# Performance work log

Measured on AMD Instinct MI355X. Metric: run time of the kernel, lower is better.

The kernel has to match this reference:

```python
import jax, jax.numpy as jnp
import numpy as np

N_NODES = 50000
EPS = 1e-5


def _gcn_edges(edge_index, num_nodes):
    # Add self loops (PyG GCNConv default) and compute symmetric normalization.
    src = jnp.concatenate([edge_index[0], jnp.arange(num_nodes, dtype=edge_index.dtype)])
    dst = jnp.concatenate([edge_index[1], jnp.arange(num_nodes, dtype=edge_index.dtype)])
    deg = jax.ops.segment_sum(jnp.ones_like(dst, dtype=jnp.float32), dst, num_segments=num_nodes)
    dinv = jnp.where(deg > 0, jax.lax.rsqrt(deg), 0.0)
    norm = dinv[src] * dinv[dst]  # [E+N]
    return src, dst, norm


def gcn_conv(x, W, b, src, dst, norm, num_nodes):
    xw = x @ W  # [N, out]
    msg = xw[src] * norm[:, None]  # [E+N, out] gather + scale
    out = jax.ops.segment_sum(msg, dst, num_segments=num_nodes)  # scatter-add
    return out + b


def layer_norm(x, g, b):
    mu = jnp.mean(x, axis=-1, keepdims=True)
    var = jnp.mean(jnp.square(x - mu), axis=-1, keepdims=True)
    return (x - mu) * jax.lax.rsqrt(var + EPS) * g + b


def setup_inputs() -> dict:
    key = jax.random.key(0)
    ks = jax.random.split(key, 12)
    d_in, d_h, d_out = 128, 128, 64
    n_edges = 800000
    x = jax.random.normal(ks[0], (N_NODES, d_in), dtype=jnp.float32)
    edge_index = jax.random.randint(ks[1], (2, n_edges), 0, N_NODES, dtype=jnp.int64)
    s = 1.0 / np.sqrt(d_in)
    return {
        "x": x,
        "edge_index": edge_index,
        "W1": jax.random.uniform(ks[2], (d_in, d_h), jnp.float32, -s, s),
        "b1": jnp.zeros((d_h,), jnp.float32),
        "W2": jax.random.uniform(ks[3], (d_h, d_h), jnp.float32, -s, s),
        "b2": jnp.zeros((d_h,), jnp.float32),
        "W3": jax.random.uniform(ks[4], (d_h, d_out), jnp.float32, -s, s),
        "b3": jnp.zeros((d_out,), jnp.float32),
        "g1": jnp.ones((d_h,), jnp.float32),
        "be1": jnp.zeros((d_h,), jnp.float32),
        "g2": jnp.ones((d_h,), jnp.float32),
        "be2": jnp.zeros((d_h,), jnp.float32),
    }


def reference(x, edge_index, W1, b1, W2, b2, W3, b3, g1, be1, g2, be2):
    num_nodes = x.shape[0]
    src, dst, norm = _gcn_edges(edge_index, num_nodes)
    h = jax.nn.relu(gcn_conv(x, W1, b1, src, dst, norm, num_nodes))
    h = layer_norm(h, g1, be1)  # dropout is identity in eval mode
    h = jax.nn.relu(gcn_conv(h, W2, b2, src, dst, norm, num_nodes))
    h = layer_norm(h, g2, be2)
    return gcn_conv(h, W3, b3, src, dst, norm, num_nodes)
```

## Files before the change

kernel.cpp:

```cpp
#include <hip/hip_runtime.h>

#define EPSV 1e-5f

typedef _Float16 half2_t __attribute__((ext_vector_type(2)));
typedef _Float16 half8_t __attribute__((ext_vector_type(8)));
typedef float float4_t __attribute__((ext_vector_type(4)));


__global__ __launch_bounds__(256) void k_fill(const int* __restrict__ src,
                                              const int* __restrict__ dst,
                                              int* __restrict__ cursor,
                                              int* __restrict__ csr, int E, int N) {
  int slice = blockIdx.x & 7;
  int lo = (int)(((long long)N * slice) >> 3);
  int hi = (int)(((long long)N * (slice + 1)) >> 3);
  int r = (blockIdx.x >> 3) * blockDim.x + threadIdx.x;
  int stride = (gridDim.x >> 3) * blockDim.x;
  for (int e = r; e < E; e += stride) {
    int d = __builtin_nontemporal_load(&dst[e]);
    if (d >= lo && d < hi) {
      int s = __builtin_nontemporal_load(&src[e]);
      int pos = atomicAdd(&cursor[d], 1);
      if (pos < 128) csr[((size_t)d << 7) + pos] = s;
    }
  }
}


__global__ __launch_bounds__(256) void k_prep(const int* __restrict__ cursor,
                                              int* __restrict__ csr,
                                              float* __restrict__ dinv,
                                              _Float16* __restrict__ ys_y,
                                              _Float16* __restrict__ ys3,
                                              int N, int N1) {
  int i = blockIdx.x * 256 + threadIdx.x;
  if (i < N) {
    int cnt = min(cursor[i], 128);
    dinv[i] = rsqrtf((float)(cnt + 1));
    int cr = (cnt + 15) & ~15;
    for (int p = cnt; p < cr; p++) csr[((size_t)i << 7) + p] = N;
  }
  if (i < 64) {
    ((half2_t*)ys_y)[((size_t)(i >> 4) * N1 + N) * 16 + (i & 15)] = (half2_t){0, 0};
  } else if (i < 96) {
    int j = i - 64;
    ((half2_t*)ys3)[((size_t)(j >> 4) * N1 + N) * 16 + (j & 15)] = (half2_t){0, 0};
  }
}


__global__ __launch_bounds__(256) void k_wprep_all(
    const float* __restrict__ W1, const float* __restrict__ W2,
    const float* __restrict__ W3, _Float16* __restrict__ Wh1,
    _Float16* __restrict__ Wh2, _Float16* __restrict__ Wh3) {
  int bid = blockIdx.x;
  const float* W;
  _Float16* Wh;
  int COLS, t;
  if (bid < 8) { W = W1; Wh = Wh1; COLS = 128; t = bid * 256 + threadIdx.x; }
  else if (bid < 16) { W = W2; Wh = Wh2; COLS = 128; t = (bid - 8) * 256 + threadIdx.x; }
  else { W = W3; Wh = Wh3; COLS = 64; t = (bid - 16) * 256 + threadIdx.x; }
  int NT = (COLS / 16) * 4 * 64;
  if (t >= NT) return;
  int lane = t & 63;
  int ks = (t >> 6) & 3;
  int nb = t >> 8;
  int col = nb * 16 + (lane & 15);
  int k0 = ks * 32 + (lane >> 4) * 8;
  half8_t v;
#pragma unroll
  for (int j = 0; j < 8; j++) v[j] = (_Float16)W[(size_t)(k0 + j) * COLS + col];
  *(half8_t*)&Wh[(size_t)t * 8] = v;
}


template <int COLS, bool LN, typename AT>
__global__ __launch_bounds__(256) void k_gemm_mfma(
    const AT* __restrict__ A, const float2* __restrict__ lnp,
    const float* __restrict__ g, const float* __restrict__ be,
    const _Float16* __restrict__ Wh, const float* __restrict__ dinv,
    _Float16* __restrict__ out, int N, int N1) {
  constexpr int NB = COLS / 16;
  int lane = threadIdx.x & 63;
  int w = threadIdx.x >> 6;
  int quad = lane >> 4;
  int mrow = blockIdx.x * 64 + w * 16 + (lane & 15);
  half8_t af[4];
  if (mrow < N) {
    if constexpr (LN) {
      float P = 0.f, Q = 0.f;
#pragma unroll
      for (int s = 0; s < 4; s++) {
        float2 pq = lnp[(size_t)s * N + mrow];
        P += pq.x; Q += pq.y;
      }
      float mean = P * (1.f / 128.f);
      float rstd = rsqrtf(Q * (1.f / 128.f) - mean * mean + EPSV);
#pragma unroll
      for (int ks = 0; ks < 4; ks++) {
        half8_t sv = *(const half8_t*)&A[((size_t)ks * N1 + mrow) * 32 + quad * 8];
        float4 g0 = *(const float4*)&g[ks * 32 + quad * 8];
        float4 g1 = *(const float4*)&g[ks * 32 + quad * 8 + 4];
        float4 e0 = *(const float4*)&be[ks * 32 + quad * 8];
        float4 e1 = *(const float4*)&be[ks * 32 + quad * 8 + 4];
        af[ks][0] = (_Float16)fmaf(((float)sv[0] - mean) * rstd, g0.x, e0.x);
        af[ks][1] = (_Float16)fmaf(((float)sv[1] - mean) * rstd, g0.y, e0.y);
        af[ks][2] = (_Float16)fmaf(((float)sv[2] - mean) * rstd, g0.z, e0.z);
        af[ks][3] = (_Float16)fmaf(((float)sv[3] - mean) * rstd, g0.w, e0.w);
        af[ks][4] = (_Float16)fmaf(((float)sv[4] - mean) * rstd, g1.x, e1.x);
        af[ks][5] = (_Float16)fmaf(((float)sv[5] - mean) * rstd, g1.y, e1.y);
        af[ks][6] = (_Float16)fmaf(((float)sv[6] - mean) * rstd, g1.z, e1.z);
        af[ks][7] = (_Float16)fmaf(((float)sv[7] - mean) * rstd, g1.w, e1.w);
      }
    } else {
      const AT* ap = A + (size_t)mrow * 128 + quad * 8;
#pragma unroll
      for (int ks = 0; ks < 4; ks++) {
        float4 f0 = *(const float4*)(ap + ks * 32);
        float4 f1 = *(const float4*)(ap + ks * 32 + 4);
        af[ks][0] = (_Float16)f0.x; af[ks][1] = (_Float16)f0.y;
        af[ks][2] = (_Float16)f0.z; af[ks][3] = (_Float16)f0.w;
        af[ks][4] = (_Float16)f1.x; af[ks][5] = (_Float16)f1.y;
        af[ks][6] = (_Float16)f1.z; af[ks][7] = (_Float16)f1.w;
      }
    }
  } else {
#pragma unroll
    for (int ks = 0; ks < 4; ks++)
#pragma unroll
      for (int j = 0; j < 8; j++) af[ks][j] = (_Float16)0.f;
  }
  float4_t acc[NB];
#pragma unroll
  for (int nb = 0; nb < NB; nb++) acc[nb] = (float4_t){0.f, 0.f, 0.f, 0.f};
#pragma unroll
  for (int nb = 0; nb < NB; nb++) {
#pragma unroll
    for (int ks = 0; ks < 4; ks++) {
      half8_t bf = *(const half8_t*)&Wh[(size_t)((nb * 4 + ks) * 64 + lane) * 8];
      acc[nb] = __builtin_amdgcn_mfma_f32_16x16x32_f16(af[ks], bf, acc[nb], 0, 0, 0);
    }
  }
  int orow0 = blockIdx.x * 64 + w * 16 + quad * 4;
#pragma unroll
  for (int r = 0; r < 4; r++) {
    int row = orow0 + r;
    if (row < N) {
      float dv = dinv[row];
#pragma unroll
      for (int nb = 0; nb < NB; nb++) {
        int dim = nb * 16 + (lane & 15);
        out[((size_t)(dim >> 5) * N1 + row) * 32 + (dim & 31)] =
            (_Float16)(acc[nb][r] * dv);
      }
    }
  }
}


__global__ __launch_bounds__(256) void k_aggs(
    const _Float16* __restrict__ ysrc, const int* __restrict__ csr,
    const int* __restrict__ cursor, const float* __restrict__ dinv,
    const float* __restrict__ b, _Float16* __restrict__ sdst,
    float2* __restrict__ lnp, int N, int N1) {
  int slice = blockIdx.x & 3;
  int lane = threadIdx.x & 63;
  int g = lane >> 4, li = lane & 15;
  int node = (blockIdx.x >> 2) * 16 + (threadIdx.x >> 6) * 4 + g;
  const half2_t* yb = (const half2_t*)ysrc + (size_t)slice * N1 * 16;
  int cnt = 0;
  if (node < N) cnt = min(cursor[node], 128);
  int cround = (cnt + 15) & ~15;
  size_t bin = (size_t)node << 7;
  float a0 = 0.f, a1 = 0.f;
  for (int c = 0; c < cround; c += 16) {
    int idx = csr[bin + c + li];
#pragma unroll
    for (int e = 0; e < 16; e++) {
      int s = __shfl(idx, (g << 4) | e, 64);
      half2_t u = yb[(size_t)s * 16 + li];
      a0 += (float)u[0];
      a1 += (float)u[1];
    }
  }
  half2_t us = yb[(size_t)min(node, N) * 16 + li];
  a0 += (float)us[0];
  a1 += (float)us[1];
  float di = (node < N) ? dinv[node] : 0.f;
  float2 bb = ((const float2*)b)[slice * 16 + li];
  float v0 = fmaxf(fmaf(a0, di, bb.x), 0.f);
  float v1 = fmaxf(fmaf(a1, di, bb.y), 0.f);
  float p = v0 + v1, q = fmaf(v0, v0, v1 * v1);
#pragma unroll
  for (int o = 1; o < 16; o <<= 1) {
    p += __shfl_xor(p, o, 64);
    q += __shfl_xor(q, o, 64);
  }
  if (node < N) {
    if (li == 0) lnp[(size_t)slice * N + node] = make_float2(p, q);
    half2_t o2;
    o2[0] = (_Float16)v0;
    o2[1] = (_Float16)v1;
    ((half2_t*)sdst)[((size_t)slice * N1 + node) * 16 + li] = o2;
  }
}


__global__ __launch_bounds__(256) void k_agg_out(
    const _Float16* __restrict__ ysrc, const int* __restrict__ csr,
    const int* __restrict__ cursor, const float* __restrict__ dinv,
    const float* __restrict__ b, float* __restrict__ out, int N, int N1) {
  int slice = blockIdx.x & 1;
  int lane = threadIdx.x & 63;
  int g = lane >> 4, li = lane & 15;
  int node = (blockIdx.x >> 1) * 16 + (threadIdx.x >> 6) * 4 + g;
  const half2_t* yb = (const half2_t*)ysrc + (size_t)slice * N1 * 16;
  int cnt = 0;
  if (node < N) cnt = min(cursor[node], 128);
  int cround = (cnt + 15) & ~15;
  size_t bin = (size_t)node << 7;
  float a0 = 0.f, a1 = 0.f;
  for (int c = 0; c < cround; c += 16) {
    int idx = csr[bin + c + li];
#pragma unroll
    for (int e = 0; e < 16; e++) {
      int s = __shfl(idx, (g << 4) | e, 64);
      half2_t u = yb[(size_t)s * 16 + li];
      a0 += (float)u[0];
      a1 += (float)u[1];
    }
  }
  if (node < N) {
    half2_t us = yb[(size_t)node * 16 + li];
    a0 += (float)us[0];
    a1 += (float)us[1];
    float di = dinv[node];
    float2 bb = ((const float2*)b)[slice * 16 + li];
    float2 o;
    o.x = fmaf(a0, di, bb.x);
    o.y = fmaf(a1, di, bb.y);
    ((float2*)out)[(size_t)node * 32 + slice * 16 + li] = o;
  }
}


extern "C" void kernel_launch(void* const* d_in, const int* in_sizes, int n_in,
                              void* d_out, int out_size, void* d_ws, size_t ws_size,
                              hipStream_t stream) {
  const float* x = (const float*)d_in[0];
  const int* ei = (const int*)d_in[1];
  const float* W1 = (const float*)d_in[2];
  const float* b1 = (const float*)d_in[3];
  const float* W2 = (const float*)d_in[4];
  const float* b2 = (const float*)d_in[5];
  const float* W3 = (const float*)d_in[6];
  const float* b3 = (const float*)d_in[7];
  const float* g1 = (const float*)d_in[8];
  const float* be1 = (const float*)d_in[9];
  const float* g2 = (const float*)d_in[10];
  const float* be2 = (const float*)d_in[11];

  int N = in_sizes[0] / 128;
  int E = in_sizes[1] / 2;
  int N1 = N + 1;
  const int* srcs = ei;
  const int* dsts = ei + E;

  char* ws = (char*)d_ws;
  size_t off = 0;
  auto alloc = [&](size_t bytes) -> char* {
    char* p = ws + off;
    off = (off + bytes + 255) & ~(size_t)255;
    return p;
  };
  float* dinv = (float*)alloc((size_t)N * 4);
  int* cursor = (int*)alloc((size_t)N * 4);
  int* csr = (int*)alloc((size_t)N * 128 * 4);
  _Float16* ys_y = (_Float16*)alloc((size_t)4 * N1 * 32 * 2);
  _Float16* ys_s = (_Float16*)alloc((size_t)4 * N1 * 32 * 2);
  _Float16* ys3 = (_Float16*)alloc((size_t)2 * N1 * 32 * 2);
  float2* lnp = (float2*)alloc((size_t)4 * N * 8);
  _Float16* Wh1 = (_Float16*)alloc(128 * 128 * 2);
  _Float16* Wh2 = (_Float16*)alloc(128 * 128 * 2);
  _Float16* Wh3 = (_Float16*)alloc(128 * 64 * 2);

  hipMemsetAsync(cursor, 0, (size_t)N * sizeof(int), stream);
  k_fill<<<2048, 256, 0, stream>>>(srcs, dsts, cursor, csr, E, N);
  k_prep<<<(N + 255) / 256, 256, 0, stream>>>(cursor, csr, dinv, ys_y, ys3, N, N1);
  k_wprep_all<<<20, 256, 0, stream>>>(W1, W2, W3, Wh1, Wh2, Wh3);

  int gb = (N + 63) / 64;
  int nb16 = (N + 15) / 16;

  k_gemm_mfma<128, false, float><<<gb, 256, 0, stream>>>(
      x, nullptr, nullptr, nullptr, Wh1, dinv, ys_y, N, N1);
  k_aggs<<<nb16 * 4, 256, 0, stream>>>(ys_y, csr, cursor, dinv, b1, ys_s, lnp, N, N1);
  k_gemm_mfma<128, true, _Float16><<<gb, 256, 0, stream>>>(
      ys_s, lnp, g1, be1, Wh2, dinv, ys_y, N, N1);
  k_aggs<<<nb16 * 4, 256, 0, stream>>>(ys_y, csr, cursor, dinv, b2, ys_s, lnp, N, N1);
  k_gemm_mfma<64, true, _Float16><<<gb, 256, 0, stream>>>(
      ys_s, lnp, g2, be2, Wh3, dinv, ys3, N, N1);
  k_agg_out<<<nb16 * 2, 256, 0, stream>>>(ys3, csr, cursor, dinv, b3,
                                          (float*)d_out, N, N1);
}
```

Baseline: 263.7 us.

## Merge prep kernels into fill and first GEMM; recompute dinv from counts

Folds the weight-conversion kernel into the CSR fill kernel and folds the padding/prep kernel into the first GEMM launch as extra blocks, cutting two launches. The dinv array is removed, and each consumer recomputes rsqrt(count+1) from the cursor array instead of loading a stored value. This trades launch overhead and one small array write/read for a little extra ALU work. There is a subtle risk: the first GEMM blocks run concurrently with the csr padding blocks, which is safe only because the GEMM does not read csr.

```diff
diff --git a/kernel.cpp b/kernel.cpp
--- a/kernel.cpp
+++ b/kernel.cpp
@@ -7,15 +7,39 @@
 typedef float float4_t __attribute__((ext_vector_type(4)));
 
 
-__global__ __launch_bounds__(256) void k_fill(const int* __restrict__ src,
-                                              const int* __restrict__ dst,
-                                              int* __restrict__ cursor,
-                                              int* __restrict__ csr, int E, int N) {
-  int slice = blockIdx.x & 7;
+__global__ __launch_bounds__(256) void k_init(
+    const float* __restrict__ W1, const float* __restrict__ W2,
+    const float* __restrict__ W3, _Float16* __restrict__ Wh1,
+    _Float16* __restrict__ Wh2, _Float16* __restrict__ Wh3,
+    const int* __restrict__ src, const int* __restrict__ dst,
+    int* __restrict__ cursor, int* __restrict__ csr, int E, int N) {
+  int bid = blockIdx.x;
+  if (bid < 20) {
+    const float* W;
+    _Float16* Wh;
+    int COLS, t;
+    if (bid < 8) { W = W1; Wh = Wh1; COLS = 128; t = bid * 256 + threadIdx.x; }
+    else if (bid < 16) { W = W2; Wh = Wh2; COLS = 128; t = (bid - 8) * 256 + threadIdx.x; }
+    else { W = W3; Wh = Wh3; COLS = 64; t = (bid - 16) * 256 + threadIdx.x; }
+    int NT = (COLS / 16) * 4 * 64;
+    if (t >= NT) return;
+    int lane = t & 63;
+    int ks = (t >> 6) & 3;
+    int nb = t >> 8;
+    int col = nb * 16 + (lane & 15);
+    int k0 = ks * 32 + (lane >> 4) * 8;
+    half8_t v;
+#pragma unroll
+    for (int j = 0; j < 8; j++) v[j] = (_Float16)W[(size_t)(k0 + j) * COLS + col];
+    *(half8_t*)&Wh[(size_t)t * 8] = v;
+    return;
+  }
+  int b = bid - 20;
+  int slice = b & 7;
   int lo = (int)(((long long)N * slice) >> 3);
   int hi = (int)(((long long)N * (slice + 1)) >> 3);
-  int r = (blockIdx.x >> 3) * blockDim.x + threadIdx.x;
-  int stride = (gridDim.x >> 3) * blockDim.x;
+  int r = (b >> 3) * 256 + threadIdx.x;
+  int stride = (2048 >> 3) * 256;
   for (int e = r; e < E; e += stride) {
     int d = __builtin_nontemporal_load(&dst[e]);
     if (d >= lo && d < hi) {
@@ -27,64 +51,17 @@
 }
 
 
-__global__ __launch_bounds__(256) void k_prep(const int* __restrict__ cursor,
-                                              int* __restrict__ csr,
-                                              float* __restrict__ dinv,
-                                              _Float16* __restrict__ ys_y,
-                                              _Float16* __restrict__ ys3,
-                                              int N, int N1) {
-  int i = blockIdx.x * 256 + threadIdx.x;
-  if (i < N) {
-    int cnt = min(cursor[i], 128);
-    dinv[i] = rsqrtf((float)(cnt + 1));
-    int cr = (cnt + 15) & ~15;
-    for (int p = cnt; p < cr; p++) csr[((size_t)i << 7) + p] = N;
-  }
-  if (i < 64) {
-    ((half2_t*)ys_y)[((size_t)(i >> 4) * N1 + N) * 16 + (i & 15)] = (half2_t){0, 0};
-  } else if (i < 96) {
-    int j = i - 64;
-    ((half2_t*)ys3)[((size_t)(j >> 4) * N1 + N) * 16 + (j & 15)] = (half2_t){0, 0};
-  }
-}
-
-
-__global__ __launch_bounds__(256) void k_wprep_all(
-    const float* __restrict__ W1, const float* __restrict__ W2,
-    const float* __restrict__ W3, _Float16* __restrict__ Wh1,
-    _Float16* __restrict__ Wh2, _Float16* __restrict__ Wh3) {
-  int bid = blockIdx.x;
-  const float* W;
-  _Float16* Wh;
-  int COLS, t;
-  if (bid < 8) { W = W1; Wh = Wh1; COLS = 128; t = bid * 256 + threadIdx.x; }
-  else if (bid < 16) { W = W2; Wh = Wh2; COLS = 128; t = (bid - 8) * 256 + threadIdx.x; }
-  else { W = W3; Wh = Wh3; COLS = 64; t = (bid - 16) * 256 + threadIdx.x; }
-  int NT = (COLS / 16) * 4 * 64;
-  if (t >= NT) return;
-  int lane = t & 63;
-  int ks = (t >> 6) & 3;
-  int nb = t >> 8;
-  int col = nb * 16 + (lane & 15);
-  int k0 = ks * 32 + (lane >> 4) * 8;
-  half8_t v;
-#pragma unroll
-  for (int j = 0; j < 8; j++) v[j] = (_Float16)W[(size_t)(k0 + j) * COLS + col];
-  *(half8_t*)&Wh[(size_t)t * 8] = v;
-}
-
-
 template <int COLS, bool LN, typename AT>
-__global__ __launch_bounds__(256) void k_gemm_mfma(
-    const AT* __restrict__ A, const float2* __restrict__ lnp,
+__device__ __forceinline__ void gemm_body(
+    int bx, const AT* __restrict__ A, const float2* __restrict__ lnp,
     const float* __restrict__ g, const float* __restrict__ be,
-    const _Float16* __restrict__ Wh, const float* __restrict__ dinv,
+    const _Float16* __restrict__ Wh, const int* __restrict__ cursor,
     _Float16* __restrict__ out, int N, int N1) {
   constexpr int NB = COLS / 16;
   int lane = threadIdx.x & 63;
   int w = threadIdx.x >> 6;
   int quad = lane >> 4;
-  int mrow = blockIdx.x * 64 + w * 16 + (lane & 15);
+  int mrow = bx * 64 + w * 16 + (lane & 15);
   half8_t af[4];
   if (mrow < N) {
     if constexpr (LN) {
@@ -141,12 +118,12 @@
       acc[nb] = __builtin_amdgcn_mfma_f32_16x16x32_f16(af[ks], bf, acc[nb], 0, 0, 0);
     }
   }
-  int orow0 = blockIdx.x * 64 + w * 16 + quad * 4;
+  int orow0 = bx * 64 + w * 16 + quad * 4;
 #pragma unroll
   for (int r = 0; r < 4; r++) {
     int row = orow0 + r;
     if (row < N) {
-      float dv = dinv[row];
+      float dv = rsqrtf((float)(min(cursor[row], 128) + 1));
 #pragma unroll
       for (int nb = 0; nb < NB; nb++) {
         int dim = nb * 16 + (lane & 15);
@@ -158,11 +135,44 @@
 }
 
 
+__global__ __launch_bounds__(256) void k_gemm1_prep(
+    const float* __restrict__ x, const _Float16* __restrict__ Wh1,
+    const int* __restrict__ cursor, int* __restrict__ csr,
+    _Float16* __restrict__ ys_y, _Float16* __restrict__ ys3,
+    int N, int N1, int gb) {
+  if ((int)blockIdx.x < gb) {
+    gemm_body<128, false, float>(blockIdx.x, x, nullptr, nullptr, nullptr, Wh1,
+                                 cursor, ys_y, N, N1);
+    return;
+  }
+  int i = (blockIdx.x - gb) * 256 + threadIdx.x;
+  if (i < N) {
+    int cnt = min(cursor[i], 128);
+    int cr = (cnt + 15) & ~15;
+    for (int p = cnt; p < cr; p++) csr[((size_t)i << 7) + p] = N;
+  }
+  if (i < 64) {
+    ((half2_t*)ys_y)[((size_t)(i >> 4) * N1 + N) * 16 + (i & 15)] = (half2_t){0, 0};
+  } else if (i < 96) {
+    int j = i - 64;
+    ((half2_t*)ys3)[((size_t)(j >> 4) * N1 + N) * 16 + (j & 15)] = (half2_t){0, 0};
+  }
+}
+
+template <int COLS, bool LN, typename AT>
+__global__ __launch_bounds__(256) void k_gemm_mfma(
+    const AT* __restrict__ A, const float2* __restrict__ lnp,
+    const float* __restrict__ g, const float* __restrict__ be,
+    const _Float16* __restrict__ Wh, const int* __restrict__ cursor,
+    _Float16* __restrict__ out, int N, int N1) {
+  gemm_body<COLS, LN, AT>(blockIdx.x, A, lnp, g, be, Wh, cursor, out, N, N1);
+}
+
+
 __global__ __launch_bounds__(256) void k_aggs(
     const _Float16* __restrict__ ysrc, const int* __restrict__ csr,
-    const int* __restrict__ cursor, const float* __restrict__ dinv,
-    const float* __restrict__ b, _Float16* __restrict__ sdst,
-    float2* __restrict__ lnp, int N, int N1) {
+    const int* __restrict__ cursor, const float* __restrict__ b,
+    _Float16* __restrict__ sdst, float2* __restrict__ lnp, int N, int N1) {
   int slice = blockIdx.x & 3;
   int lane = threadIdx.x & 63;
   int g = lane >> 4, li = lane & 15;
@@ -186,7 +196,7 @@
   half2_t us = yb[(size_t)min(node, N) * 16 + li];
   a0 += (float)us[0];
   a1 += (float)us[1];
-  float di = (node < N) ? dinv[node] : 0.f;
+  float di = rsqrtf((float)(cnt + 1));
   float2 bb = ((const float2*)b)[slice * 16 + li];
   float v0 = fmaxf(fmaf(a0, di, bb.x), 0.f);
   float v1 = fmaxf(fmaf(a1, di, bb.y), 0.f);
@@ -208,8 +218,8 @@
 
 __global__ __launch_bounds__(256) void k_agg_out(
     const _Float16* __restrict__ ysrc, const int* __restrict__ csr,
-    const int* __restrict__ cursor, const float* __restrict__ dinv,
-    const float* __restrict__ b, float* __restrict__ out, int N, int N1) {
+    const int* __restrict__ cursor, const float* __restrict__ b,
+    float* __restrict__ out, int N, int N1) {
   int slice = blockIdx.x & 1;
   int lane = threadIdx.x & 63;
   int g = lane >> 4, li = lane & 15;
@@ -234,7 +244,7 @@
     half2_t us = yb[(size_t)node * 16 + li];
     a0 += (float)us[0];
     a1 += (float)us[1];
-    float di = dinv[node];
+    float di = rsqrtf((float)(cnt + 1));
     float2 bb = ((const float2*)b)[slice * 16 + li];
     float2 o;
     o.x = fmaf(a0, di, bb.x);
@@ -273,7 +283,6 @@
     off = (off + bytes + 255) & ~(size_t)255;
     return p;
   };
-  float* dinv = (float*)alloc((size_t)N * 4);
   int* cursor = (int*)alloc((size_t)N * 4);
   int* csr = (int*)alloc((size_t)N * 128 * 4);
   _Float16* ys_y = (_Float16*)alloc((size_t)4 * N1 * 32 * 2);
@@ -284,22 +293,21 @@
   _Float16* Wh2 = (_Float16*)alloc(128 * 128 * 2);
   _Float16* Wh3 = (_Float16*)alloc(128 * 64 * 2);
 
+  int gb = (N + 63) / 64;
+  int pb = (N + 255) / 256;
+  int nb16 = (N + 15) / 16;
+
   hipMemsetAsync(cursor, 0, (size_t)N * sizeof(int), stream);
-  k_fill<<<2048, 256, 0, stream>>>(srcs, dsts, cursor, csr, E, N);
-  k_prep<<<(N + 255) / 256, 256, 0, stream>>>(cursor, csr, dinv, ys_y, ys3, N, N1);
-  k_wprep_all<<<20, 256, 0, stream>>>(W1, W2, W3, Wh1, Wh2, Wh3);
-
-  int gb = (N + 63) / 64;
-  int nb16 = (N + 15) / 16;
-
-  k_gemm_mfma<128, false, float><<<gb, 256, 0, stream>>>(
-      x, nullptr, nullptr, nullptr, Wh1, dinv, ys_y, N, N1);
-  k_aggs<<<nb16 * 4, 256, 0, stream>>>(ys_y, csr, cursor, dinv, b1, ys_s, lnp, N, N1);
+  k_init<<<2068, 256, 0, stream>>>(W1, W2, W3, Wh1, Wh2, Wh3,
+                                   srcs, dsts, cursor, csr, E, N);
+  k_gemm1_prep<<<gb + pb, 256, 0, stream>>>(x, Wh1, cursor, csr, ys_y, ys3,
+                                            N, N1, gb);
+  k_aggs<<<nb16 * 4, 256, 0, stream>>>(ys_y, csr, cursor, b1, ys_s, lnp, N, N1);
   k_gemm_mfma<128, true, _Float16><<<gb, 256, 0, stream>>>(
-      ys_s, lnp, g1, be1, Wh2, dinv, ys_y, N, N1);
-  k_aggs<<<nb16 * 4, 256, 0, stream>>>(ys_y, csr, cursor, dinv, b2, ys_s, lnp, N, N1);
+      ys_s, lnp, g1, be1, Wh2, cursor, ys_y, N, N1);
+  k_aggs<<<nb16 * 4, 256, 0, stream>>>(ys_y, csr, cursor, b2, ys_s, lnp, N, N1);
   k_gemm_mfma<64, true, _Float16><<<gb, 256, 0, stream>>>(
-      ys_s, lnp, g2, be2, Wh3, dinv, ys3, N, N1);
-  k_agg_out<<<nb16 * 2, 256, 0, stream>>>(ys3, csr, cursor, dinv, b3,
+      ys_s, lnp, g2, be2, Wh3, cursor, ys3, N, N1);
+  k_agg_out<<<nb16 * 2, 256, 0, stream>>>(ys3, csr, cursor, b3,
                                           (float*)d_out, N, N1);
 }
```

New measurement: 258.7 us. Within noise of the previous version (-1.9%).
